# Optimization experiments

Measured on AMD Instinct MI355X. Metric: run time of the kernel, lower is better.

## Reference

```python
import jax, jax.numpy as jnp
import numpy as np

N_NODES = 50000
N_EDGES = 1600000
IN_DIM, HID, OUT = 128, 64, 32


def _glorot(key, fan_in, fan_out):
    s = 1.0 / np.sqrt(fan_in)
    return jax.random.uniform(key, (fan_in, fan_out), jnp.float32, -s, s)


def setup_inputs() -> dict:
    key = jax.random.key(0)
    ks = jax.random.split(key, 12)
    x = jax.random.normal(ks[0], (N_NODES, IN_DIM), jnp.float32)
    edge_index = jax.random.randint(ks[1], (2, N_EDGES), 0, N_NODES, jnp.int32)
    inp = {"x": x, "edge_index": edge_index}
    # 4 SAGEConv layers: (in->hid), (hid->hid), (hid->hid), (hid->hid)
    dims = [(IN_DIM, HID), (HID, HID), (HID, HID), (HID, HID)]
    names = ["1a", "1b", "2a", "2b"]
    for i, ((di, do), nm) in enumerate(zip(dims, names)):
        k1, k2 = jax.random.split(ks[2 + i])
        inp[f"W{nm}_l"] = _glorot(k1, di, do)       # neighbor transform (with bias)
        inp[f"b{nm}"] = jnp.zeros((do,), jnp.float32)
        inp[f"W{nm}_r"] = _glorot(k2, di, do)       # root/self transform (no bias)
    inp["Wlin"] = _glorot(ks[10], HID, OUT)
    inp["blin"] = jnp.zeros((OUT,), jnp.float32)
    return inp


def _sage(h, src, dst, Wl, bl, Wr, n_nodes):
    # SAGEConv: out = mean_{j in N(i)} x_j @ Wl + bl + x_i @ Wr
    msg = h[src]                                                    # [E, D] gather
    ssum = jax.ops.segment_sum(msg, dst, num_segments=n_nodes)     # [N, D] scatter-add
    cnt = jax.ops.segment_sum(jnp.ones((src.shape[0], 1), h.dtype), dst, num_segments=n_nodes)
    agg = ssum / jnp.maximum(cnt, 1.0)                              # mean; 0 for isolated nodes
    return agg @ Wl + bl + h @ Wr


def reference(x, edge_index, W1a_l, b1a, W1a_r, W1b_l, b1b, W1b_r,
              W2a_l, b2a, W2a_r, W2b_l, b2b, W2b_r, Wlin, blin):
    src, dst = edge_index[0], edge_index[1]
    n = x.shape[0]
    # conv1 = GraphSAGE(2 layers): sage -> relu -> sage ; then outer F.relu
    h = jax.nn.relu(_sage(x, src, dst, W1a_l, b1a, W1a_r, n))
    h = jax.nn.relu(_sage(h, src, dst, W1b_l, b1b, W1b_r, n))
    # conv2 = GraphSAGE(2 layers): sage -> relu -> sage (no final act)
    h = jax.nn.relu(_sage(h, src, dst, W2a_l, b2a, W2a_r, n))
    h = _sage(h, src, dst, W2b_l, b2b, W2b_r, n)
    return h @ Wlin + blin
```

## Files before the change

### kernel.cpp

```cpp
#include <hip/hip_runtime.h>
#include <hip/hip_fp16.h>


#define CHUNK 4096
#define EPT 16
#define SLICE_W 512
#define MAXS 128

__global__ __launch_bounds__(256) void bucket_scatter_direct(
    const int* __restrict__ e32, int* __restrict__ scnt,
    unsigned* __restrict__ bedge, int E, int S, int bcap)
{
    __shared__ int h[MAXS];
    __shared__ int hb[MAXS];
    const int tid = threadIdx.x, b = blockIdx.x;
    for (int i = tid; i < S; i += 256) h[i] = 0;
    __syncthreads();
    const int lo = b * CHUNK;
    unsigned v[EPT];
    int sl[EPT], rk[EPT];
    #pragma unroll
    for (int k = 0; k < EPT; ++k) {
        const int e = lo + k * 256 + tid;
        sl[k] = -1;
        if (e < E) {
            const int s = e32[e], d = e32[E + e];
            v[k]  = ((unsigned)s << 16) | (unsigned)d;
            sl[k] = d >> 9;
            rk[k] = atomicAdd(&h[sl[k]], 1);
        }
    }
    __syncthreads();
    for (int i = tid; i < S; i += 256)
        hb[i] = h[i] ? atomicAdd(&scnt[i], h[i]) : 0;
    __syncthreads();
    #pragma unroll
    for (int k = 0; k < EPT; ++k) {
        if (sl[k] >= 0) {
            const int pos = hb[sl[k]] + rk[k];
            if (pos < bcap)
                bedge[(size_t)sl[k] * bcap + pos] = v[k];
        }
    }
}

__global__ __launch_bounds__(1024) void csr_fill2(
    const unsigned* __restrict__ bedge, const int* __restrict__ scnt,
    int* __restrict__ rbeg, int* __restrict__ deg,
    float* __restrict__ inv, unsigned short* __restrict__ adj,
    int N, int bcap)
{
    __shared__ int cnt[SLICE_W];
    __shared__ int sc[SLICE_W];
    const int s = blockIdx.x, tid = threadIdx.x;
    const int n = min(scnt[s], bcap);
    const size_t base = (size_t)s * bcap;
    if (tid < SLICE_W) cnt[tid] = 0;
    __syncthreads();
    for (int i = tid; i < n; i += 1024)
        atomicAdd(&cnt[bedge[base + i] & (SLICE_W - 1)], 1);
    __syncthreads();
    if (tid < SLICE_W) sc[tid] = cnt[tid];
    __syncthreads();
    for (int off = 1; off < SLICE_W; off <<= 1) {
        int a = 0;
        if (tid < SLICE_W && tid >= off) a = sc[tid - off];
        __syncthreads();
        if (tid < SLICE_W) sc[tid] += a;
        __syncthreads();
    }
    if (tid < SLICE_W) {
        const int c = cnt[tid];
        const int excl = sc[tid] - c;
        const int node = (s << 9) + tid;
        if (node < N) {
            rbeg[node] = (int)base + excl;
            deg[node]  = c;
            inv[node]  = 1.0f / (float)(c > 0 ? c : 1);
        }
        cnt[tid] = excl;
    }
    __syncthreads();
    for (int i = tid; i < n; i += 1024) {
        const unsigned v = bedge[base + i];
        const int p = atomicAdd(&cnt[v & (SLICE_W - 1)], 1);
        adj[base + p] = (unsigned short)(v >> 16);
    }
}

template<bool RELU>
__global__ __launch_bounds__(256) void gather_fused(
    const __half* __restrict__ t, const unsigned short* __restrict__ adj,
    const int* __restrict__ rbeg, const int* __restrict__ deg,
    const float* __restrict__ inv, const __half* __restrict__ u,
    float* __restrict__ out, int N)
{
    const int node = (blockIdx.x * 256 + threadIdx.x) >> 6;
    const int lane = threadIdx.x & 63;
    const int grp  = lane >> 3;
    const int d0   = (lane & 7) * 8;
    if (node >= N) return;
    const int beg = rbeg[node];
    const int end = beg + deg[node];
    float a[8] = {0.f, 0.f, 0.f, 0.f, 0.f, 0.f, 0.f, 0.f};
    int j = beg + grp;
    for (; j + 8 < end; j += 16) {
        const int n0 = adj[j], n1 = adj[j + 8];
        const float4 p0 = *(const float4*)(t + (size_t)n0 * 64 + d0);
        const float4 p1 = *(const float4*)(t + (size_t)n1 * 64 + d0);
        const __half2* h0 = (const __half2*)&p0;
        const __half2* h1 = (const __half2*)&p1;
        #pragma unroll
        for (int k = 0; k < 4; ++k) {
            float2 f0 = __half22float2(h0[k]);
            float2 f1 = __half22float2(h1[k]);
            a[2 * k]     += f0.x + f1.x;
            a[2 * k + 1] += f0.y + f1.y;
        }
    }
    if (j < end) {
        const float4 p0 = *(const float4*)(t + (size_t)adj[j] * 64 + d0);
        const __half2* h0 = (const __half2*)&p0;
        #pragma unroll
        for (int k = 0; k < 4; ++k) {
            float2 f0 = __half22float2(h0[k]);
            a[2 * k]     += f0.x;
            a[2 * k + 1] += f0.y;
        }
    }
    #pragma unroll
    for (int k = 0; k < 8; ++k) {
        a[k] += __shfl_xor(a[k], 8);
        a[k] += __shfl_xor(a[k], 16);
        a[k] += __shfl_xor(a[k], 32);
    }
    if (grp == 0) {
        const float vi = inv[node];
        const float4 uv = *(const float4*)(u + (size_t)node * 64 + d0);
        const __half2* uh = (const __half2*)&uv;
        float4 o0, o1;
        {
            float2 g0 = __half22float2(uh[0]);
            float2 g1 = __half22float2(uh[1]);
            float2 g2 = __half22float2(uh[2]);
            float2 g3 = __half22float2(uh[3]);
            o0.x = g0.x + a[0] * vi; o0.y = g0.y + a[1] * vi;
            o0.z = g1.x + a[2] * vi; o0.w = g1.y + a[3] * vi;
            o1.x = g2.x + a[4] * vi; o1.y = g2.y + a[5] * vi;
            o1.z = g3.x + a[6] * vi; o1.w = g3.y + a[7] * vi;
        }
        if (RELU) {
            o0.x = fmaxf(o0.x, 0.f); o0.y = fmaxf(o0.y, 0.f);
            o0.z = fmaxf(o0.z, 0.f); o0.w = fmaxf(o0.w, 0.f);
            o1.x = fmaxf(o1.x, 0.f); o1.y = fmaxf(o1.y, 0.f);
            o1.z = fmaxf(o1.z, 0.f); o1.w = fmaxf(o1.w, 0.f);
        }
        *(float4*)(out + (size_t)node * 64 + d0)     = o0;
        *(float4*)(out + (size_t)node * 64 + d0 + 4) = o1;
    }
}

template<int K>
__global__ __launch_bounds__(256) void mm_dual(
    const float* __restrict__ A, const float* __restrict__ Wl,
    const float* __restrict__ Wr, const float* __restrict__ bias,
    __half* __restrict__ T, __half* __restrict__ U, int M)
{
    __shared__ float As[64][36];
    __shared__ float Wls[32 * 64];
    __shared__ float Wrs[32 * 64];
    const int tid  = threadIdx.x;
    const int row0 = blockIdx.x * 64;
    const int tx = tid & 15, ty = tid >> 4;
    float accT[4][4] = {{0.f}}, accU[4][4] = {{0.f}};

    for (int kc = 0; kc < K; kc += 32) {
        if (kc) __syncthreads();
        for (int i = tid * 4; i < 64 * 32; i += 1024) {
            int r = i >> 5, c = i & 31;
            int gr = row0 + r;
            float4 v = make_float4(0.f, 0.f, 0.f, 0.f);
            if (gr < M) v = *(const float4*)&A[(size_t)gr * K + kc + c];
            *(float4*)&As[r][c] = v;
        }
        for (int i = tid * 4; i < 32 * 64; i += 1024) {
            *(float4*)&Wls[i] = *(const float4*)&Wl[kc * 64 + i];
            *(float4*)&Wrs[i] = *(const float4*)&Wr[kc * 64 + i];
        }
        __syncthreads();
        #pragma unroll 4
        for (int kk = 0; kk < 32; ++kk) {
            float a[4];
            #pragma unroll
            for (int r = 0; r < 4; ++r) a[r] = As[ty * 4 + r][kk];
            float bl[4], br[4];
            #pragma unroll
            for (int c = 0; c < 4; ++c) {
                bl[c] = Wls[kk * 64 + tx * 4 + c];
                br[c] = Wrs[kk * 64 + tx * 4 + c];
            }
            #pragma unroll
            for (int r = 0; r < 4; ++r)
                #pragma unroll
                for (int c = 0; c < 4; ++c) {
                    accT[r][c] += a[r] * bl[c];
                    accU[r][c] += a[r] * br[c];
                }
        }
    }

    const float4 bv = *(const float4*)&bias[tx * 4];
    #pragma unroll
    for (int r = 0; r < 4; ++r) {
        int gr = row0 + ty * 4 + r;
        if (gr >= M) continue;
        union { int2 v; __half2 h[2]; } tp;
        tp.h[0] = __floats2half2_rn(accT[r][0], accT[r][1]);
        tp.h[1] = __floats2half2_rn(accT[r][2], accT[r][3]);
        *(int2*)&T[(size_t)gr * 64 + tx * 4] = tp.v;
        union { int2 v; __half2 h[2]; } up;
        up.h[0] = __floats2half2_rn(accU[r][0] + bv.x, accU[r][1] + bv.y);
        up.h[1] = __floats2half2_rn(accU[r][2] + bv.z, accU[r][3] + bv.w);
        *(int2*)&U[(size_t)gr * 64 + tx * 4] = up.v;
    }
}

__global__ __launch_bounds__(256) void mm_lin(
    const float* __restrict__ A, const float* __restrict__ W,
    const float* __restrict__ bias, float* __restrict__ C, int M)
{
    __shared__ float As[64][68];
    __shared__ float Ws[64 * 32];
    const int tid  = threadIdx.x;
    const int row0 = blockIdx.x * 64;

    for (int i = tid * 4; i < 64 * 32; i += 1024) {
        *(float4*)&Ws[i] = *(const float4*)&W[i];
    }
    for (int i = tid * 4; i < 64 * 64; i += 1024) {
        int r = i >> 6, c = i & 63;
        int gr = row0 + r;
        float4 v = make_float4(0.f, 0.f, 0.f, 0.f);
        if (gr < M) v = *(const float4*)&A[(size_t)gr * 64 + c];
        *(float4*)&As[r][c] = v;
    }
    __syncthreads();

    const int tx = tid & 15, ty = tid >> 4;
    float acc[4][2] = {{0.f}};
    #pragma unroll 4
    for (int kk = 0; kk < 64; ++kk) {
        float a[4];
        #pragma unroll
        for (int r = 0; r < 4; ++r) a[r] = As[ty * 4 + r][kk];
        float b0 = Ws[kk * 32 + tx * 2];
        float b1 = Ws[kk * 32 + tx * 2 + 1];
        #pragma unroll
        for (int r = 0; r < 4; ++r) {
            acc[r][0] += a[r] * b0;
            acc[r][1] += a[r] * b1;
        }
    }
    #pragma unroll
    for (int r = 0; r < 4; ++r) {
        int gr = row0 + ty * 4 + r;
        if (gr >= M) continue;
        float2 o = make_float2(acc[r][0] + bias[tx * 2],
                               acc[r][1] + bias[tx * 2 + 1]);
        *(float2*)&C[(size_t)gr * 32 + tx * 2] = o;
    }
}

extern "C" void kernel_launch(void* const* d_in, const int* in_sizes, int n_in,
                              void* d_out, int out_size, void* d_ws, size_t ws_size,
                              hipStream_t stream) {
    const float* x     = (const float*)d_in[0];
    const int*   ei    = (const int*)  d_in[1];
    const float* W1a_l = (const float*)d_in[2];
    const float* b1a   = (const float*)d_in[3];
    const float* W1a_r = (const float*)d_in[4];
    const float* W1b_l = (const float*)d_in[5];
    const float* b1b   = (const float*)d_in[6];
    const float* W1b_r = (const float*)d_in[7];
    const float* W2a_l = (const float*)d_in[8];
    const float* b2a   = (const float*)d_in[9];
    const float* W2a_r = (const float*)d_in[10];
    const float* W2b_l = (const float*)d_in[11];
    const float* b2b   = (const float*)d_in[12];
    const float* W2b_r = (const float*)d_in[13];
    const float* Wlin  = (const float*)d_in[14];
    const float* blin  = (const float*)d_in[15];

    const int N = in_sizes[0] / 128;
    const int E = in_sizes[1] / 2;
    const int S = (N + SLICE_W - 1) / SLICE_W;
    const int B = (E + CHUNK - 1) / CHUNK;
    const int bcap = (((E + S - 1) / S) + 2048 + 15) & ~15;

    size_t o = 0;
    auto take = [&](size_t bytes) -> void* {
        void* p = (char*)d_ws + o;
        o += (bytes + 255) & ~(size_t)255;
        return p;
    };
    int*            scnt  = (int*)     take((size_t)S * 4);
    unsigned*       bedge = (unsigned*)take((size_t)S * bcap * 4);
    int*            rbeg  = (int*)     take((size_t)N * 4);
    int*            deg   = (int*)     take((size_t)N * 4);
    float*          inv   = (float*)   take((size_t)N * 4);
    unsigned short* adj   = (unsigned short*)take((size_t)S * bcap * 2);
    __half*         t     = (__half*)  take((size_t)N * 64 * 2);
    __half*         u     = (__half*)  take((size_t)N * 64 * 2);
    float*          hA    = (float*)   take((size_t)N * 64 * 4);
    float*          hB    = (float*)   take((size_t)N * 64 * 4);
    (void)ws_size; (void)n_in; (void)out_size;

    const int mb = (N + 63) / 64;
    const int gb = (N * 64 + 255) / 256;

    hipMemsetAsync(scnt, 0, (size_t)S * 4, stream);
    bucket_scatter_direct<<<B, 256, 0, stream>>>(ei, scnt, bedge, E, S, bcap);
    csr_fill2<<<S, 1024, 0, stream>>>(bedge, scnt, rbeg, deg, inv, adj, N, bcap);

    mm_dual<128><<<mb, 256, 0, stream>>>(x, W1a_l, W1a_r, b1a, t, u, N);
    gather_fused<true><<<gb, 256, 0, stream>>>(t, adj, rbeg, deg, inv, u, hA, N);
    mm_dual<64><<<mb, 256, 0, stream>>>(hA, W1b_l, W1b_r, b1b, t, u, N);
    gather_fused<true><<<gb, 256, 0, stream>>>(t, adj, rbeg, deg, inv, u, hB, N);
    mm_dual<64><<<mb, 256, 0, stream>>>(hB, W2a_l, W2a_r, b2a, t, u, N);
    gather_fused<true><<<gb, 256, 0, stream>>>(t, adj, rbeg, deg, inv, u, hA, N);
    mm_dual<64><<<mb, 256, 0, stream>>>(hA, W2b_l, W2b_r, b2b, t, u, N);
    gather_fused<false><<<gb, 256, 0, stream>>>(t, adj, rbeg, deg, inv, u, hB, N);
    mm_lin<<<mb, 256, 0, stream>>>(hB, Wlin, blin, (float*)d_out, N);
}
```

Before: 265.4 us.

## Fold final linear layer into last SAGE layer weights via precomposition

Because the last SAGE layer has no activation, its two weight matrices and bias are composed with Wlin (and blin) in a tiny single-block kernel. The final mm_dual then produces 32-wide outputs directly and a new 32-wide gather writes the result to the output buffer. This removes the separate mm_lin kernel and halves the per-edge gather width and bytes of the last aggregation. Precomposing weights changes rounding order, and the fp16 t/u intermediates now carry the already-projected values.

```diff
diff --git a/kernel.cpp b/kernel.cpp
--- a/kernel.cpp
+++ b/kernel.cpp
@@ -85,6 +85,37 @@
         const unsigned v = bedge[base + i];
         const int p = atomicAdd(&cnt[v & (SLICE_W - 1)], 1);
         adj[base + p] = (unsigned short)(v >> 16);
+    }
+}
+
+__global__ __launch_bounds__(256) void compose(
+    const float* __restrict__ Wl, const float* __restrict__ Wr,
+    const float* __restrict__ b2, const float* __restrict__ Wlin,
+    const float* __restrict__ blin, float* __restrict__ C1,
+    float* __restrict__ C2, float* __restrict__ cb)
+{
+    __shared__ float Ws[64 * 32];
+    const int tid = threadIdx.x;
+    for (int i = tid * 4; i < 64 * 32; i += 1024)
+        *(float4*)&Ws[i] = *(const float4*)&Wlin[i];
+    __syncthreads();
+    for (int idx = tid; idx < 64 * 32; idx += 256) {
+        const int r = idx >> 5, c = idx & 31;
+        float s1 = 0.f, s2 = 0.f;
+        #pragma unroll 8
+        for (int k = 0; k < 64; ++k) {
+            const float w = Ws[k * 32 + c];
+            s1 += Wl[r * 64 + k] * w;
+            s2 += Wr[r * 64 + k] * w;
+        }
+        C1[idx] = s1;
+        C2[idx] = s2;
+    }
+    if (tid < 32) {
+        float s = blin[tid];
+        #pragma unroll 8
+        for (int k = 0; k < 64; ++k) s += b2[k] * Ws[k * 32 + tid];
+        cb[tid] = s;
     }
 }
 
@@ -160,19 +191,88 @@
     }
 }
 
-template<int K>
+__global__ __launch_bounds__(256) void gather32(
+    const __half* __restrict__ t, const unsigned short* __restrict__ adj,
+    const int* __restrict__ rbeg, const int* __restrict__ deg,
+    const float* __restrict__ inv, const __half* __restrict__ u,
+    float* __restrict__ out, int N)
+{
+    const int node = (blockIdx.x * 256 + threadIdx.x) >> 6;
+    const int lane = threadIdx.x & 63;
+    const int grp  = lane >> 2;
+    const int d0   = (lane & 3) * 8;
+    if (node >= N) return;
+    const int beg = rbeg[node];
+    const int end = beg + deg[node];
+    float a[8] = {0.f, 0.f, 0.f, 0.f, 0.f, 0.f, 0.f, 0.f};
+    int j = beg + grp;
+    for (; j + 16 < end; j += 32) {
+        const int n0 = adj[j], n1 = adj[j + 16];
+        const float4 p0 = *(const float4*)(t + (size_t)n0 * 32 + d0);
+        const float4 p1 = *(const float4*)(t + (size_t)n1 * 32 + d0);
+        const __half2* h0 = (const __half2*)&p0;
+        const __half2* h1 = (const __half2*)&p1;
+        #pragma unroll
+        for (int k = 0; k < 4; ++k) {
+            float2 f0 = __half22float2(h0[k]);
+            float2 f1 = __half22float2(h1[k]);
+            a[2 * k]     += f0.x + f1.x;
+            a[2 * k + 1] += f0.y + f1.y;
+        }
+    }
+    if (j < end) {
+        const float4 p0 = *(const float4*)(t + (size_t)adj[j] * 32 + d0);
+        const __half2* h0 = (const __half2*)&p0;
+        #pragma unroll
+        for (int k = 0; k < 4; ++k) {
+            float2 f0 = __half22float2(h0[k]);
+            a[2 * k]     += f0.x;
+            a[2 * k + 1] += f0.y;
+        }
+    }
+    #pragma unroll
+    for (int k = 0; k < 8; ++k) {
+        a[k] += __shfl_xor(a[k], 4);
+        a[k] += __shfl_xor(a[k], 8);
+        a[k] += __shfl_xor(a[k], 16);
+        a[k] += __shfl_xor(a[k], 32);
+    }
+    if (grp == 0) {
+        const float vi = inv[node];
+        const float4 uv = *(const float4*)(u + (size_t)node * 32 + d0);
+        const __half2* uh = (const __half2*)&uv;
+        float4 o0, o1;
+        float2 g0 = __half22float2(uh[0]);
+        float2 g1 = __half22float2(uh[1]);
+        float2 g2 = __half22float2(uh[2]);
+        float2 g3 = __half22float2(uh[3]);
+        o0.x = g0.x + a[0] * vi; o0.y = g0.y + a[1] * vi;
+        o0.z = g1.x + a[2] * vi; o0.w = g1.y + a[3] * vi;
+        o1.x = g2.x + a[4] * vi; o1.y = g2.y + a[5] * vi;
+        o1.z = g3.x + a[6] * vi; o1.w = g3.y + a[7] * vi;
+        *(float4*)(out + (size_t)node * 32 + d0)     = o0;
+        *(float4*)(out + (size_t)node * 32 + d0 + 4) = o1;
+    }
+}
+
+template<int K, int DOUT>
 __global__ __launch_bounds__(256) void mm_dual(
     const float* __restrict__ A, const float* __restrict__ Wl,
     const float* __restrict__ Wr, const float* __restrict__ bias,
     __half* __restrict__ T, __half* __restrict__ U, int M)
 {
+    constexpr int CT = DOUT / 16;
     __shared__ float As[64][36];
-    __shared__ float Wls[32 * 64];
-    __shared__ float Wrs[32 * 64];
+    __shared__ float Wls[32 * DOUT];
+    __shared__ float Wrs[32 * DOUT];
     const int tid  = threadIdx.x;
     const int row0 = blockIdx.x * 64;
     const int tx = tid & 15, ty = tid >> 4;
-    float accT[4][4] = {{0.f}}, accU[4][4] = {{0.f}};
+    float accT[4][CT], accU[4][CT];
+    #pragma unroll
+    for (int r = 0; r < 4; ++r)
+        #pragma unroll
+        for (int c = 0; c < CT; ++c) { accT[r][c] = 0.f; accU[r][c] = 0.f; }
 
     for (int kc = 0; kc < K; kc += 32) {
         if (kc) __syncthreads();
@@ -183,9 +283,9 @@
             if (gr < M) v = *(const float4*)&A[(size_t)gr * K + kc + c];
             *(float4*)&As[r][c] = v;
         }
-        for (int i = tid * 4; i < 32 * 64; i += 1024) {
-            *(float4*)&Wls[i] = *(const float4*)&Wl[kc * 64 + i];
-            *(float4*)&Wrs[i] = *(const float4*)&Wr[kc * 64 + i];
+        for (int i = tid * 4; i < 32 * DOUT; i += 1024) {
+            *(float4*)&Wls[i] = *(const float4*)&Wl[kc * DOUT + i];
+            *(float4*)&Wrs[i] = *(const float4*)&Wr[kc * DOUT + i];
         }
         __syncthreads();
         #pragma unroll 4
@@ -193,81 +293,46 @@
             float a[4];
             #pragma unroll
             for (int r = 0; r < 4; ++r) a[r] = As[ty * 4 + r][kk];
-            float bl[4], br[4];
+            float bl[CT], br[CT];
             #pragma unroll
-            for (int c = 0; c < 4; ++c) {
-                bl[c] = Wls[kk * 64 + tx * 4 + c];
-                br[c] = Wrs[kk * 64 + tx * 4 + c];
+            for (int c = 0; c < CT; ++c) {
+                bl[c] = Wls[kk * DOUT + tx * CT + c];
+                br[c] = Wrs[kk * DOUT + tx * CT + c];
             }
             #pragma unroll
             for (int r = 0; r < 4; ++r)
                 #pragma unroll
-                for (int c = 0; c < 4; ++c) {
+                for (int c = 0; c < CT; ++c) {
                     accT[r][c] += a[r] * bl[c];
                     accU[r][c] += a[r] * br[c];
                 }
         }
     }
 
-    const float4 bv = *(const float4*)&bias[tx * 4];
+    float bv[CT];
+    #pragma unroll
+    for (int c = 0; c < CT; ++c) bv[c] = bias[tx * CT + c];
     #pragma unroll
     for (int r = 0; r < 4; ++r) {
         int gr = row0 + ty * 4 + r;
         if (gr >= M) continue;
-        union { int2 v; __half2 h[2]; } tp;
-        tp.h[0] = __floats2half2_rn(accT[r][0], accT[r][1]);
-        tp.h[1] = __floats2half2_rn(accT[r][2], accT[r][3]);
-        *(int2*)&T[(size_t)gr * 64 + tx * 4] = tp.v;
-        union { int2 v; __half2 h[2]; } up;
-        up.h[0] = __floats2half2_rn(accU[r][0] + bv.x, accU[r][1] + bv.y);
-        up.h[1] = __floats2half2_rn(accU[r][2] + bv.z, accU[r][3] + bv.w);
-        *(int2*)&U[(size_t)gr * 64 + tx * 4] = up.v;
-    }
-}
-
-__global__ __launch_bounds__(256) void mm_lin(
-    const float* __restrict__ A, const float* __restrict__ W,
-    const float* __restrict__ bias, float* __restrict__ C, int M)
-{
-    __shared__ float As[64][68];
-    __shared__ float Ws[64 * 32];
-    const int tid  = threadIdx.x;
-    const int row0 = blockIdx.x * 64;
-
-    for (int i = tid * 4; i < 64 * 32; i += 1024) {
-        *(float4*)&Ws[i] = *(const float4*)&W[i];
-    }
-    for (int i = tid * 4; i < 64 * 64; i += 1024) {
-        int r = i >> 6, c = i & 63;
-        int gr = row0 + r;
-        float4 v = make_float4(0.f, 0.f, 0.f, 0.f);
-        if (gr < M) v = *(const float4*)&A[(size_t)gr * 64 + c];
-        *(float4*)&As[r][c] = v;
-    }
-    __syncthreads();
-
-    const int tx = tid & 15, ty = tid >> 4;
-    float acc[4][2] = {{0.f}};
-    #pragma unroll 4
-    for (int kk = 0; kk < 64; ++kk) {
-        float a[4];
-        #pragma unroll
-        for (int r = 0; r < 4; ++r) a[r] = As[ty * 4 + r][kk];
-        float b0 = Ws[kk * 32 + tx * 2];
-        float b1 = Ws[kk * 32 + tx * 2 + 1];
-        #pragma unroll
-        for (int r = 0; r < 4; ++r) {
-            acc[r][0] += a[r] * b0;
-            acc[r][1] += a[r] * b1;
-        }
-    }
-    #pragma unroll
-    for (int r = 0; r < 4; ++r) {
-        int gr = row0 + ty * 4 + r;
-        if (gr >= M) continue;
-        float2 o = make_float2(acc[r][0] + bias[tx * 2],
-                               acc[r][1] + bias[tx * 2 + 1]);
-        *(float2*)&C[(size_t)gr * 32 + tx * 2] = o;
+        if (CT == 4) {
+            union { int2 v; __half2 h[2]; } tp;
+            tp.h[0] = __floats2half2_rn(accT[r][0], accT[r][1]);
+            tp.h[1] = __floats2half2_rn(accT[r][2], accT[r][3]);
+            *(int2*)&T[(size_t)gr * DOUT + tx * 4] = tp.v;
+            union { int2 v; __half2 h[2]; } up;
+            up.h[0] = __floats2half2_rn(accU[r][0] + bv[0], accU[r][1] + bv[1]);
+            up.h[1] = __floats2half2_rn(accU[r][2] + bv[2], accU[r][3] + bv[3]);
+            *(int2*)&U[(size_t)gr * DOUT + tx * 4] = up.v;
+        } else {
+            union { int v; __half2 h; } tp;
+            tp.h = __floats2half2_rn(accT[r][0], accT[r][1]);
+            *(int*)&T[(size_t)gr * DOUT + tx * 2] = tp.v;
+            union { int v; __half2 h; } up;
+            up.h = __floats2half2_rn(accU[r][0] + bv[0], accU[r][1] + bv[1]);
+            *(int*)&U[(size_t)gr * DOUT + tx * 2] = up.v;
+        }
     }
 }
 
@@ -313,6 +378,9 @@
     __half*         u     = (__half*)  take((size_t)N * 64 * 2);
     float*          hA    = (float*)   take((size_t)N * 64 * 4);
     float*          hB    = (float*)   take((size_t)N * 64 * 4);
+    float*          C1    = (float*)   take((size_t)64 * 32 * 4);
+    float*          C2    = (float*)   take((size_t)64 * 32 * 4);
+    float*          cb    = (float*)   take((size_t)32 * 4);
     (void)ws_size; (void)n_in; (void)out_size;
 
     const int mb = (N + 63) / 64;
@@ -321,14 +389,14 @@
     hipMemsetAsync(scnt, 0, (size_t)S * 4, stream);
     bucket_scatter_direct<<<B, 256, 0, stream>>>(ei, scnt, bedge, E, S, bcap);
     csr_fill2<<<S, 1024, 0, stream>>>(bedge, scnt, rbeg, deg, inv, adj, N, bcap);
-
-    mm_dual<128><<<mb, 256, 0, stream>>>(x, W1a_l, W1a_r, b1a, t, u, N);
+    compose<<<1, 256, 0, stream>>>(W2b_l, W2b_r, b2b, Wlin, blin, C1, C2, cb);
+
+    mm_dual<128, 64><<<mb, 256, 0, stream>>>(x, W1a_l, W1a_r, b1a, t, u, N);
     gather_fused<true><<<gb, 256, 0, stream>>>(t, adj, rbeg, deg, inv, u, hA, N);
-    mm_dual<64><<<mb, 256, 0, stream>>>(hA, W1b_l, W1b_r, b1b, t, u, N);
+    mm_dual<64, 64><<<mb, 256, 0, stream>>>(hA, W1b_l, W1b_r, b1b, t, u, N);
     gather_fused<true><<<gb, 256, 0, stream>>>(t, adj, rbeg, deg, inv, u, hB, N);
-    mm_dual<64><<<mb, 256, 0, stream>>>(hB, W2a_l, W2a_r, b2a, t, u, N);
+    mm_dual<64, 64><<<mb, 256, 0, stream>>>(hB, W2a_l, W2a_r, b2a, t, u, N);
     gather_fused<true><<<gb, 256, 0, stream>>>(t, adj, rbeg, deg, inv, u, hA, N);
-    mm_dual<64><<<mb, 256, 0, stream>>>(hA, W2b_l, W2b_r, b2b, t, u, N);
-    gather_fused<false><<<gb, 256, 0, stream>>>(t, adj, rbeg, deg, inv, u, hB, N);
-    mm_lin<<<mb, 256, 0, stream>>>(hB, Wlin, blin, (float*)d_out, N);
-}
+    mm_dual<64, 32><<<mb, 256, 0, stream>>>(hA, C1, C2, cb, t, u, N);
+    gather32<<<gb, 256, 0, stream>>>(t, adj, rbeg, deg, inv, u, (float*)d_out, N);
+}
```

Result: faster. 256.6 us, median of 2 (-3.3%).
